# Kernel tuning notes

Measured on AMD Instinct MI355X. Metric: run time of the kernel, lower is better.

The kernel has to match this reference:

```python
import jax, jax.numpy as jnp
import numpy as np

B, H, W, CIN, F, KH, KW, E = 16, 112, 112, 128, 256, 3, 3, 3


@jax.custom_vjp
def ste_sign(x):
    # larq-style ste_sign: sign with sign(0) -> +1
    return jnp.where(x >= 0, 1.0, -1.0).astype(x.dtype)

def _ste_fwd(x):
    return ste_sign(x), x

def _ste_bwd(x, g):
    # straight-through estimator, clipped to |x| <= 1
    return (g * (jnp.abs(x) <= 1).astype(g.dtype),)

ste_sign.defvjp(_ste_fwd, _ste_bwd)


def conv2d(x, k):
    return jax.lax.conv_general_dilated(
        x, k, window_strides=(1, 1), padding='VALID',
        dimension_numbers=('NHWC', 'HWIO', 'NHWC'))


def setup_inputs() -> dict:
    key = jax.random.key(0)
    k1, k2 = jax.random.split(key)
    x = jax.random.normal(k1, (B, H, W, CIN), dtype=jnp.float32)
    kernels = jax.random.normal(k2, (E, KH, KW, CIN, F), dtype=jnp.float32) * 0.1
    # alpha initialized as mean |kernel| per output filter (as in build())
    alphas = jnp.mean(jnp.abs(kernels), axis=(1, 2, 3))  # [E, F]
    return {"x": x, "kernels": kernels, "alphas": alphas}


def reference(x, kernels, alphas):
    kh, kw, cin = kernels.shape[1], kernels.shape[2], kernels.shape[3]
    D = kh * kw * cin  # db_dimension
    xq = ste_sign(x)  # binarized input (shared across estimators)
    ones_k = jnp.ones((kh, kw, cin, 1), dtype=x.dtype)
    # beta: box-filter of |x| over window and channels, divided by D -> [B,H',W']
    beta = conv2d(jnp.abs(x), ones_k)[..., 0] / D
    out = jnp.zeros((1,), dtype=x.dtype)  # broadcast accumulator
    for e in range(kernels.shape[0]):
        Z = conv2d(xq, ste_sign(kernels[e]))  # [B,H',W',F], binary conv
        K = beta[..., None] * alphas[e]       # outer(beta, alpha)
        out = out + Z * K
    return out
```

## Files before the change

kernel.cpp:

```cpp
#include <hip/hip_runtime.h>
#include <hip/hip_bf16.h>
#include <stdint.h>

#define B_   16
#define H_   112
#define W_   112
#define CIN  128
#define F_   256
#define OH   110
#define OW   110
#define MTOT (B_*OH*OW)
#define KTOT 1152
#define PIX_IN (B_*H_*W_)
#define D_INV (1.0f/1152.0f)

typedef float floatx4 __attribute__((ext_vector_type(4)));
typedef int   intx4   __attribute__((ext_vector_type(4)));

typedef __attribute__((address_space(1))) uint32_t guint;
typedef __attribute__((address_space(3))) uint32_t luint;

__device__ __forceinline__ void gld_lds16(const void* g, void* l) {
    __builtin_amdgcn_global_load_lds((guint*)g, (luint*)l, 16, 0, 0);
}

#define WST_OFF   0
#define SF_OFF    294912
#define S_OFF     295936
#define BETA_OFF  1098752
#define XQ_OFF    1873152
#define NEED_FULL (XQ_OFF + (size_t)PIX_IN*CIN)

__global__ void prep_wq(const float* __restrict__ kern, const float* __restrict__ alph,
                        int8_t* __restrict__ wst, float* __restrict__ sf) {
    int idx = blockIdx.x * 256 + threadIdx.x;
    int r = idx >> 8, f = idx & 255;
    float a0 = alph[f], a1 = alph[256 + f], a2 = alph[512 + f];
    float w = 0.f;
    float kv0 = kern[idx], kv1 = kern[294912 + idx], kv2 = kern[589824 + idx];
    w += (__float_as_uint(kv0) & 0x80000000u) ? -a0 : a0;
    w += (__float_as_uint(kv1) & 0x80000000u) ? -a1 : a1;
    w += (__float_as_uint(kv2) & 0x80000000u) ? -a2 : a2;
    float s = (a0 + a1 + a2) * (1.0f / 127.0f);
    int q = (int)__builtin_rintf(w / s);
    wst[((((r >> 6) * 2 + (f >> 7)) * 4 + ((r >> 4) & 3)) * 128 + (f & 127)) * 16 + (r & 15)]
        = (int8_t)q;
    if (r == 0) sf[f] = s;
}

__device__ __forceinline__ uint32_t pack4sign(float4 v) {
    uint32_t b0 = ((__float_as_uint(v.x) >> 31) * 0xFEu) ^ 0x01u;
    uint32_t b1 = ((__float_as_uint(v.y) >> 31) * 0xFEu) ^ 0x01u;
    uint32_t b2 = ((__float_as_uint(v.z) >> 31) * 0xFEu) ^ 0x01u;
    uint32_t b3 = ((__float_as_uint(v.w) >> 31) * 0xFEu) ^ 0x01u;
    return b0 | (b1 << 8) | (b2 << 16) | (b3 << 24);
}

__global__ void prep_x(const float* __restrict__ x, uint32_t* __restrict__ xq,
                       float* __restrict__ S, int write_xq) {
    int idx = blockIdx.x * 256 + threadIdx.x;
    float4 v = ((const float4*)x)[idx];
    if (write_xq) xq[idx] = pack4sign(v);
    float s = fabsf(v.x) + fabsf(v.y) + fabsf(v.z) + fabsf(v.w);
#pragma unroll
    for (int o = 1; o < 32; o <<= 1) s += __shfl_xor(s, o, 64);
    if ((threadIdx.x & 31) == 0) S[idx >> 5] = s;
}

__global__ void prep_beta(const float* __restrict__ S, float* __restrict__ beta) {
    int m = blockIdx.x * 256 + threadIdx.x;
    if (m >= MTOT) return;
    int b = m / (OH * OW); int r = m - b * (OH * OW);
    int oi = r / OW, oj = r - oi * OW;
    const float* sp = S + (b * H_ + oi) * W_ + oj;
    float acc = 0.f;
#pragma unroll
    for (int dh = 0; dh < 3; ++dh)
#pragma unroll
        for (int dw = 0; dw < 3; ++dw) acc += sp[dh * W_ + dw];
    beta[m] = acc * D_INV;
}

template <bool PREBIN>
__global__ __launch_bounds__(256)
void conv_main(const void* __restrict__ xin, const int8_t* __restrict__ wst,
               const float* __restrict__ sf, const float* __restrict__ beta,
               float* __restrict__ out) {
    __shared__ char smem[16384];

    const int t = threadIdx.x;
    const int l = t & 63, wv = t >> 6;
    const int quad = l >> 4, lane16 = l & 15;
    const int wm = wv >> 1, wn = wv & 1;
    const int f0 = blockIdx.x * 128;
    const int m0 = blockIdx.y * 128;

    const char* a_base[2];
    const char* b_base[2];
#pragma unroll
    for (int q = 0; q < 2; ++q) {
        int idx = q * 256 + t;
        int chunk = idx >> 7, rn = idx & 127;
        int m = m0 + rn; if (m >= MTOT) m = MTOT - 1;
        int b = m / (OH * OW); int rr = m - b * (OH * OW);
        int oi = rr / OW, oj = rr - oi * OW;
        long pix = ((long)(b * H_ + oi) * W_ + oj) * CIN;
        a_base[q] = (const char*)xin + (PREBIN ? (pix + chunk * 16)
                                               : (pix + chunk * 16) * 4);
        b_base[q] = (const char*)wst + blockIdx.x * 8192 + idx * 16;
    }

    intx4 acc[4][4];
#pragma unroll
    for (int a = 0; a < 4; ++a)
#pragma unroll
        for (int bb = 0; bb < 4; ++bb) acc[a][bb] = (intx4){0, 0, 0, 0};

    for (int ks = 0; ks < 18; ++ks) {
        int kh = ks / 6, rem = ks - kh * 6;
        int kw = rem >> 1, c0 = (rem & 1) << 6;
        int aoff = (kh * W_ + kw) * CIN + c0;
#pragma unroll
        for (int q = 0; q < 2; ++q) {
            int idx = q * 256 + t;
            if (PREBIN) {
                gld_lds16(a_base[q] + aoff, smem + idx * 16);
            } else {
                const float4* src = (const float4*)(a_base[q] + (long)aoff * 4);
                float4 v0 = src[0], v1 = src[1], v2 = src[2], v3 = src[3];
                uint4 pv = make_uint4(pack4sign(v0), pack4sign(v1),
                                      pack4sign(v2), pack4sign(v3));
                *(uint4*)(smem + idx * 16) = pv;
            }
            gld_lds16(b_base[q] + (long)ks * 16384, smem + 8192 + idx * 16);
        }
        __syncthreads();

        intx4 af[4], bf[4];
#pragma unroll
        for (int tm = 0; tm < 4; ++tm) {
            int row = wm * 64 + tm * 16 + lane16;
            af[tm] = *(const intx4*)(smem + quad * 2048 + row * 16);
        }
#pragma unroll
        for (int tn = 0; tn < 4; ++tn) {
            int col = wn * 64 + tn * 16 + lane16;
            bf[tn] = *(const intx4*)(smem + 8192 + quad * 2048 + col * 16);
        }
#pragma unroll
        for (int tm = 0; tm < 4; ++tm)
#pragma unroll
            for (int tn = 0; tn < 4; ++tn)
                acc[tm][tn] = __builtin_amdgcn_mfma_i32_16x16x64_i8(
                    af[tm], bf[tn], acc[tm][tn], 0, 0, 0);
        __syncthreads();
    }

    float sv[4];
#pragma unroll
    for (int tn = 0; tn < 4; ++tn) sv[tn] = sf[f0 + wn * 64 + tn * 16 + lane16];

#pragma unroll
    for (int tm = 0; tm < 4; ++tm) {
#pragma unroll
        for (int i = 0; i < 4; ++i) {
            int m = m0 + wm * 64 + tm * 16 + quad * 4 + i;
            if (m < MTOT) {
                float bv = beta[m];
                float* op = out + (long)m * F_ + f0 + wn * 64 + lane16;
#pragma unroll
                for (int tn = 0; tn < 4; ++tn)
                    op[tn * 16] = (float)acc[tm][tn][i] * (bv * sv[tn]);
            }
        }
    }
}

extern "C" void kernel_launch(void* const* d_in, const int* in_sizes, int n_in,
                              void* d_out, int out_size, void* d_ws, size_t ws_size,
                              hipStream_t stream) {
    const float* x    = (const float*)d_in[0];
    const float* kern = (const float*)d_in[1];
    const float* alph = (const float*)d_in[2];
    float* out = (float*)d_out;
    char* ws = (char*)d_ws;

    int8_t* wst  = (int8_t*)(ws + WST_OFF);
    float*  sf   = (float*)(ws + SF_OFF);
    float*  S    = (float*)(ws + S_OFF);
    float*  beta = (float*)(ws + BETA_OFF);
    char*   xq   = ws + XQ_OFF;
    bool prebin = ws_size >= NEED_FULL;

    hipLaunchKernelGGL(prep_wq, dim3(KTOT * F_ / 256), dim3(256), 0, stream,
                       kern, alph, wst, sf);
    hipLaunchKernelGGL(prep_x, dim3(PIX_IN * CIN / 4 / 256), dim3(256), 0, stream,
                       x, (uint32_t*)xq, S, (int)prebin);
    hipLaunchKernelGGL(prep_beta, dim3((MTOT + 255) / 256), dim3(256), 0, stream, S, beta);

    dim3 grid(2, (MTOT + 127) / 128);
    if (prebin)
        hipLaunchKernelGGL(conv_main<true>, grid, dim3(256), 0, stream,
                           (const void*)xq, wst, sf, beta, out);
    else
        hipLaunchKernelGGL(conv_main<false>, grid, dim3(256), 0, stream,
                           (const void*)x, wst, sf, beta, out);
}
```

Before: 352.2 us.

## Stage input row window in LDS once and stream weights from registers

The conv kernel now tiles output per image: each block loads a 5-row by 112-column window of binarized input into padded LDS once (stride 136 to avoid bank conflicts), then indexes all 9 filter taps from that window instead of re-gathering an im2col A tile per k-step. Weight fragments are read directly from global memory into registers with a two-step-ahead rotating prefetch, so the per-step __syncthreads and LDS staging of B go away. This removes the redundant input reloads and barriers, at the cost of roughly 76KB of LDS per block (limiting occupancy) and a serial prologue load before any MFMA work.

```diff
diff --git a/kernel.cpp b/kernel.cpp
--- a/kernel.cpp
+++ b/kernel.cpp
@@ -9,20 +9,16 @@
 #define F_   256
 #define OH   110
 #define OW   110
-#define MTOT (B_*OH*OW)
+#define TPI  (OH*OW)
+#define MTOT (B_*TPI)
 #define KTOT 1152
 #define PIX_IN (B_*H_*W_)
 #define D_INV (1.0f/1152.0f)
-
-typedef float floatx4 __attribute__((ext_vector_type(4)));
-typedef int   intx4   __attribute__((ext_vector_type(4)));
-
-typedef __attribute__((address_space(1))) uint32_t guint;
-typedef __attribute__((address_space(3))) uint32_t luint;
-
-__device__ __forceinline__ void gld_lds16(const void* g, void* l) {
-    __builtin_amdgcn_global_load_lds((guint*)g, (luint*)l, 16, 0, 0);
-}
+#define TILES_PER_IMG 95
+#define WSTR 136
+#define WIN_BYTES (5*112*WSTR)
+
+typedef int intx4 __attribute__((ext_vector_type(4)));
 
 #define WST_OFF   0
 #define SF_OFF    294912
@@ -70,7 +66,7 @@
 __global__ void prep_beta(const float* __restrict__ S, float* __restrict__ beta) {
     int m = blockIdx.x * 256 + threadIdx.x;
     if (m >= MTOT) return;
-    int b = m / (OH * OW); int r = m - b * (OH * OW);
+    int b = m / TPI; int r = m - b * TPI;
     int oi = r / OW, oj = r - oi * OW;
     const float* sp = S + (b * H_ + oi) * W_ + oj;
     float acc = 0.f;
@@ -82,33 +78,57 @@
 }
 
 template <bool PREBIN>
-__global__ __launch_bounds__(256)
+__global__ __launch_bounds__(256, 2)
 void conv_main(const void* __restrict__ xin, const int8_t* __restrict__ wst,
                const float* __restrict__ sf, const float* __restrict__ beta,
                float* __restrict__ out) {
-    __shared__ char smem[16384];
+    __shared__ char smem[WIN_BYTES];
 
     const int t = threadIdx.x;
     const int l = t & 63, wv = t >> 6;
     const int quad = l >> 4, lane16 = l & 15;
     const int wm = wv >> 1, wn = wv & 1;
     const int f0 = blockIdx.x * 128;
-    const int m0 = blockIdx.y * 128;
-
-    const char* a_base[2];
-    const char* b_base[2];
-#pragma unroll
-    for (int q = 0; q < 2; ++q) {
-        int idx = q * 256 + t;
-        int chunk = idx >> 7, rn = idx & 127;
-        int m = m0 + rn; if (m >= MTOT) m = MTOT - 1;
-        int b = m / (OH * OW); int rr = m - b * (OH * OW);
-        int oi = rr / OW, oj = rr - oi * OW;
-        long pix = ((long)(b * H_ + oi) * W_ + oj) * CIN;
-        a_base[q] = (const char*)xin + (PREBIN ? (pix + chunk * 16)
-                                               : (pix + chunk * 16) * 4);
-        b_base[q] = (const char*)wst + blockIdx.x * 8192 + idx * 16;
-    }
+    const int img = blockIdx.y / TILES_PER_IMG;
+    const int tile = blockIdx.y - img * TILES_PER_IMG;
+    const int p0 = tile * 128;
+    const int oi0 = p0 / OW;
+
+    if (PREBIN) {
+        const char* xi = (const char*)xin + (size_t)img * (H_ * W_ * CIN);
+        for (int i = t; i < 4480; i += 256) {
+            int pix = i >> 3, chunk = i & 7;
+            int wr = pix / 112, wc = pix - wr * 112;
+            int gr = oi0 + wr; if (gr > 111) gr = 111;
+            uint4 v = *(const uint4*)(xi + ((gr * W_ + wc) * CIN + chunk * 16));
+            *(uint4*)(smem + pix * WSTR + chunk * 16) = v;
+        }
+    } else {
+        const float* xi = (const float*)xin + (size_t)img * (H_ * W_ * CIN);
+        for (int i = t; i < 4480; i += 256) {
+            int pix = i >> 3, chunk = i & 7;
+            int wr = pix / 112, wc = pix - wr * 112;
+            int gr = oi0 + wr; if (gr > 111) gr = 111;
+            const float4* s = (const float4*)(xi + (gr * W_ + wc) * CIN + chunk * 16);
+            uint4 pv = make_uint4(pack4sign(s[0]), pack4sign(s[1]),
+                                  pack4sign(s[2]), pack4sign(s[3]));
+            *(uint4*)(smem + pix * WSTR + chunk * 16) = pv;
+        }
+    }
+
+    int abase[4];
+#pragma unroll
+    for (int tm = 0; tm < 4; ++tm) {
+        int p = p0 + wm * 64 + tm * 16 + lane16;
+        if (p > TPI - 1) p = TPI - 1;
+        int oi = p / OW, oj = p - oi * OW;
+        abase[tm] = ((oi - oi0) * 112 + oj) * WSTR + quad * 16;
+    }
+
+    const char* bbase = (const char*)wst + blockIdx.x * 8192 + quad * 2048
+                        + (wn * 64 + lane16) * 16;
+
+    __syncthreads();
 
     intx4 acc[4][4];
 #pragma unroll
@@ -116,58 +136,53 @@
 #pragma unroll
         for (int bb = 0; bb < 4; ++bb) acc[a][bb] = (intx4){0, 0, 0, 0};
 
-    for (int ks = 0; ks < 18; ++ks) {
-        int kh = ks / 6, rem = ks - kh * 6;
-        int kw = rem >> 1, c0 = (rem & 1) << 6;
-        int aoff = (kh * W_ + kw) * CIN + c0;
-#pragma unroll
-        for (int q = 0; q < 2; ++q) {
-            int idx = q * 256 + t;
-            if (PREBIN) {
-                gld_lds16(a_base[q] + aoff, smem + idx * 16);
-            } else {
-                const float4* src = (const float4*)(a_base[q] + (long)aoff * 4);
-                float4 v0 = src[0], v1 = src[1], v2 = src[2], v3 = src[3];
-                uint4 pv = make_uint4(pack4sign(v0), pack4sign(v1),
-                                      pack4sign(v2), pack4sign(v3));
-                *(uint4*)(smem + idx * 16) = pv;
-            }
-            gld_lds16(b_base[q] + (long)ks * 16384, smem + 8192 + idx * 16);
-        }
-        __syncthreads();
-
-        intx4 af[4], bf[4];
-#pragma unroll
-        for (int tm = 0; tm < 4; ++tm) {
-            int row = wm * 64 + tm * 16 + lane16;
-            af[tm] = *(const intx4*)(smem + quad * 2048 + row * 16);
-        }
-#pragma unroll
-        for (int tn = 0; tn < 4; ++tn) {
-            int col = wn * 64 + tn * 16 + lane16;
-            bf[tn] = *(const intx4*)(smem + 8192 + quad * 2048 + col * 16);
-        }
+    intx4 b0[4], b1[4], b2[4];
+#pragma unroll
+    for (int tn = 0; tn < 4; ++tn) {
+        b0[tn] = *(const intx4*)(bbase + tn * 256);
+        b1[tn] = *(const intx4*)(bbase + 16384 + tn * 256);
+    }
+
+    auto step = [&](int ks, intx4 (&bc)[4], intx4 (&bp)[4]) {
+        int ksp = ks + 2; if (ksp > 17) ksp = 0;
+#pragma unroll
+        for (int tn = 0; tn < 4; ++tn)
+            bp[tn] = *(const intx4*)(bbase + ksp * 16384 + tn * 256);
+        int kh = (ks * 171) >> 10;
+        int rem = ks - kh * 6;
+        int aoff = (kh * 112 + (rem >> 1)) * WSTR + (rem & 1) * 64;
+        intx4 af[4];
+#pragma unroll
+        for (int tm = 0; tm < 4; ++tm)
+            af[tm] = *(const intx4*)(smem + abase[tm] + aoff);
 #pragma unroll
         for (int tm = 0; tm < 4; ++tm)
 #pragma unroll
             for (int tn = 0; tn < 4; ++tn)
                 acc[tm][tn] = __builtin_amdgcn_mfma_i32_16x16x64_i8(
-                    af[tm], bf[tn], acc[tm][tn], 0, 0, 0);
-        __syncthreads();
+                    af[tm], bc[tn], acc[tm][tn], 0, 0, 0);
+    };
+
+    for (int kb = 0; kb < 18; kb += 3) {
+        step(kb + 0, b0, b2);
+        step(kb + 1, b1, b0);
+        step(kb + 2, b2, b1);
     }
 
     float sv[4];
 #pragma unroll
     for (int tn = 0; tn < 4; ++tn) sv[tn] = sf[f0 + wn * 64 + tn * 16 + lane16];
 
+    const size_t mbase = (size_t)img * TPI;
 #pragma unroll
     for (int tm = 0; tm < 4; ++tm) {
 #pragma unroll
         for (int i = 0; i < 4; ++i) {
-            int m = m0 + wm * 64 + tm * 16 + quad * 4 + i;
-            if (m < MTOT) {
+            int p = p0 + wm * 64 + tm * 16 + quad * 4 + i;
+            if (p < TPI) {
+                size_t m = mbase + p;
                 float bv = beta[m];
-                float* op = out + (long)m * F_ + f0 + wn * 64 + lane16;
+                float* op = out + m * F_ + f0 + wn * 64 + lane16;
 #pragma unroll
                 for (int tn = 0; tn < 4; ++tn)
                     op[tn * 16] = (float)acc[tm][tn][i] * (bv * sv[tn]);
@@ -198,7 +213,7 @@
                        x, (uint32_t*)xq, S, (int)prebin);
     hipLaunchKernelGGL(prep_beta, dim3((MTOT + 255) / 256), dim3(256), 0, stream, S, beta);
 
-    dim3 grid(2, (MTOT + 127) / 128);
+    dim3 grid(2, B_ * TILES_PER_IMG);
     if (prebin)
         hipLaunchKernelGGL(conv_main<true>, grid, dim3(256), 0, stream,
                            (const void*)xq, wst, sf, beta, out);
```

Result: slower. 360.8 us (+2.5%).
